# Performance work log

Measured on AMD Instinct MI355X. Metric: run time of the kernel, lower is better.

## Reference

```python
import jax, jax.numpy as jnp
import numpy as np

B, S, H = 2, 1024, 2048
NH, NKV, HD = 16, 4, 128
KB = 1024
THETA = 10000.0
NREP = NH // NKV
NEG = -1e9


def rotate_half(x):
    x1, x2 = x[..., : HD // 2], x[..., HD // 2 :]
    return jnp.concatenate((-x2, x1), axis=-1)


def setup_inputs() -> dict:
    key = jax.random.key(0)
    ks = jax.random.split(key, 9)
    wscale = 1.0 / np.sqrt(H)
    hidden_states = jax.random.normal(ks[0], (B, S, H), dtype=jnp.float32)
    # causal additive mask over the self-attention block only
    causal = jnp.tril(jnp.ones((S, S), dtype=bool))
    attention_mask = jnp.where(causal, 0.0, NEG).astype(jnp.float32)
    attention_mask = jnp.broadcast_to(attention_mask[None, None], (B, 1, S, S))
    position_ids = jnp.broadcast_to(jnp.arange(S, dtype=jnp.int32)[None], (B, S))
    kb_keys = jax.random.normal(ks[1], (B, KB, NKV * HD), dtype=jnp.float32)
    kb_values = jax.random.normal(ks[2], (B, KB, NKV * HD), dtype=jnp.float32)
    Wq = jax.random.normal(ks[3], (NH * HD, H), dtype=jnp.float32) * wscale
    Wq_new = jax.random.normal(ks[4], (NH * HD, H), dtype=jnp.float32) * wscale
    Wk = jax.random.normal(ks[5], (NKV * HD, H), dtype=jnp.float32) * wscale
    Wv = jax.random.normal(ks[6], (NKV * HD, H), dtype=jnp.float32) * wscale
    Wo = jax.random.normal(ks[7], (H, NH * HD), dtype=jnp.float32) * wscale
    return {
        'hidden_states': hidden_states, 'attention_mask': attention_mask,
        'position_ids': position_ids, 'kb_keys': kb_keys, 'kb_values': kb_values,
        'Wq': Wq, 'Wq_new': Wq_new, 'Wk': Wk, 'Wv': Wv, 'Wo': Wo,
    }


def _rope(position_ids, dtype):
    inv_freq = 1.0 / (THETA ** (jnp.arange(0, HD, 2, dtype=jnp.float32) / HD))
    freqs = position_ids.astype(jnp.float32)[:, :, None] * inv_freq[None, None, :]  # (B,S,HD/2)
    emb = jnp.concatenate((freqs, freqs), axis=-1)  # (B,S,HD)
    return jnp.cos(emb).astype(dtype)[:, None], jnp.sin(emb).astype(dtype)[:, None]  # (B,1,S,HD)


def reference(hidden_states, attention_mask, position_ids, kb_keys, kb_values,
              Wq, Wq_new, Wk, Wv, Wo):
    x = hidden_states
    q = jnp.einsum('bsh,dh->bsd', x, Wq).reshape(B, S, NH, HD).transpose(0, 2, 1, 3)
    q_new = jnp.einsum('bsh,dh->bsd', x, Wq_new).reshape(B, S, NH, HD).transpose(0, 2, 1, 3)
    k = jnp.einsum('bsh,dh->bsd', x, Wk).reshape(B, S, NKV, HD).transpose(0, 2, 1, 3)
    v = jnp.einsum('bsh,dh->bsd', x, Wv).reshape(B, S, NKV, HD).transpose(0, 2, 1, 3)

    cos, sin = _rope(position_ids, x.dtype)
    q = q * cos + rotate_half(q) * sin          # roped self queries
    k = k * cos + rotate_half(k) * sin          # roped self keys; q_new / KB keys stay un-roped

    # GQA repeat of KV heads
    k = jnp.repeat(k, NREP, axis=1)             # (B,NH,S,HD)
    v = jnp.repeat(v, NREP, axis=1)
    kb_k = jnp.repeat(kb_keys.reshape(B, KB, NKV, HD).transpose(0, 2, 1, 3), NREP, axis=1)   # (B,NH,KB,HD)
    kb_v = jnp.repeat(kb_values.reshape(B, KB, NKV, HD).transpose(0, 2, 1, 3), NREP, axis=1)

    scale = 1.0 / np.sqrt(HD)
    scores_kb = jnp.einsum('bhqd,bhkd->bhqk', q_new, kb_k) * scale      # (B,NH,S,KB)
    scores_self = jnp.einsum('bhqd,bhkd->bhqk', q, k) * scale + attention_mask  # (B,NH,S,S)
    scores = jnp.concatenate((scores_kb, scores_self), axis=-1)          # (B,NH,S,KB+S)
    attn = jax.nn.softmax(scores, axis=-1)

    v_full = jnp.concatenate((kb_v, v), axis=2)                          # (B,NH,KB+S,HD)
    out = jnp.einsum('bhqk,bhkd->bhqd', attn, v_full)                    # (B,NH,S,HD)
    out = out.transpose(0, 2, 1, 3).reshape(B, S, NH * HD)
    return jnp.einsum('bsd,hd->bsh', out, Wo)
```

## Files before the change

kernel.cpp:

```cpp
#include <hip/hip_runtime.h>

#define Bc   2
#define Sc   1024
#define Hc   2048
#define NHc  16
#define NKVc 4
#define HDc  128
#define KBc  1024
#define NREPc 4

typedef unsigned short ushort_t;
typedef unsigned int uint32;
typedef __attribute__((ext_vector_type(8))) __bf16 bf16x8;
typedef __attribute__((ext_vector_type(4))) float f32x4;

static __device__ __forceinline__ size_t dsz(int x) { return (size_t)x; }

static __device__ __forceinline__ ushort_t f2bf(float f) {
  uint32 u = __float_as_uint(f);
  u += 0x7fffu + ((u >> 16) & 1u);
  return (ushort_t)(u >> 16);
}
static __device__ __forceinline__ float bf2f(ushort_t u) {
  return __uint_as_float(((uint32)u) << 16);
}

#define ROPE_INV 0.14391156831212787f
#define QSCALE   (0.08838834764831845f * 1.4426950408889634f)

#define FSEG 1048576
__global__ void conv_all(const float* __restrict__ x,  const float* __restrict__ Wq,
                         const float* __restrict__ Wqn, const float* __restrict__ Wk,
                         const float* __restrict__ Wv,  const float* __restrict__ Wo,
                         ushort_t* xb, ushort_t* Wqb, ushort_t* Wqnb,
                         ushort_t* Wkb, ushort_t* Wvb, ushort_t* Wob)
{
  int i = blockIdx.x * 256 + threadIdx.x;
  const float* s; ushort_t* d; int off;
  if      (i <     FSEG)            { s = x;   d = xb;   off = i; }
  else if (i < 2 * FSEG)            { s = Wq;  d = Wqb;  off = i - FSEG; }
  else if (i < 3 * FSEG)            { s = Wqn; d = Wqnb; off = i - 2 * FSEG; }
  else if (i < 3 * FSEG + FSEG / 4) { s = Wk;  d = Wkb;  off = i - 3 * FSEG; }
  else if (i < 3 * FSEG + FSEG / 2) { s = Wv;  d = Wvb;  off = i - 3 * FSEG - FSEG / 4; }
  else                              { s = Wo;  d = Wob;  off = i - 3 * FSEG - FSEG / 2; }
  float4 v = ((const float4*)s)[off];
  ushort4 o;
  o.x = f2bf(v.x); o.y = f2bf(v.y); o.z = f2bf(v.z); o.w = f2bf(v.w);
  ((ushort4*)d)[off] = o;
}

#define GL16(gsrc, ldst)                                                \
  __builtin_amdgcn_global_load_lds(                                     \
      (const __attribute__((address_space(1))) void*)(gsrc),            \
      (__attribute__((address_space(3))) void*)(ldst), 16, 0, 0)

__global__ __launch_bounds__(256) void gemm_proj(
    const ushort_t* __restrict__ A,
    const ushort_t* __restrict__ Wqb,  const ushort_t* __restrict__ Wqnb,
    const ushort_t* __restrict__ Wkb,  const ushort_t* __restrict__ Wvb,
    ushort_t* __restrict__ qb, ushort_t* __restrict__ qnb,
    ushort_t* __restrict__ kkvb, ushort_t* __restrict__ vkvb)
{
  __shared__ ushort_t sA[128 * 32];
  __shared__ ushort_t sB[128 * 32];

  const int K = Hc;
  const int bx = blockIdx.x;
  const ushort_t* Bseg; ushort_t* Cseg; int segN, colseg; float scale;
  if      (bx < 16) { Bseg = Wqb;  Cseg = qb;   segN = 2048; colseg = bx * 128;        scale = 1.f; }
  else if (bx < 32) { Bseg = Wqnb; Cseg = qnb;  segN = 2048; colseg = (bx - 16) * 128; scale = QSCALE; }
  else if (bx < 36) { Bseg = Wkb;  Cseg = kkvb; segN = 512;  colseg = (bx - 32) * 128; scale = 1.f; }
  else              { Bseg = Wvb;  Cseg = vkvb; segN = 512;  colseg = (bx - 36) * 128; scale = 1.f; }

  const int tid  = threadIdx.x;
  const int lane = tid & 63;
  const int wid  = tid >> 6;
  const int wr   = wid >> 1;
  const int wc   = wid & 1;
  const int row0 = blockIdx.y * 128;
  const int fr = lane & 15;
  const int fq = lane >> 4;

  f32x4 acc[4][4];
  #pragma unroll
  for (int m = 0; m < 4; ++m)
    #pragma unroll
    for (int n = 0; n < 4; ++n) acc[m][n] = (f32x4){0.f, 0.f, 0.f, 0.f};

  const int rS = tid >> 2;
  const int kg = (tid & 3) * 8;
  const ushort_t* Asrc0 = A + dsz(row0 + rS) * K + kg;
  const ushort_t* Asrc1 = A + dsz(row0 + 64 + rS) * K + kg;
  const ushort_t* Bsrc0 = Bseg + dsz(colseg + rS) * K + kg;
  const ushort_t* Bsrc1 = Bseg + dsz(colseg + 64 + rS) * K + kg;
  char* ldsA0 = (char*)sA + tid * 16;
  char* ldsA1 = (char*)sA + 4096 + tid * 16;
  char* ldsB0 = (char*)sB + tid * 16;
  char* ldsB1 = (char*)sB + 4096 + tid * 16;

  for (int k0 = 0; k0 < K; k0 += 32) {
    GL16(Asrc0 + k0, ldsA0);
    GL16(Asrc1 + k0, ldsA1);
    GL16(Bsrc0 + k0, ldsB0);
    GL16(Bsrc1 + k0, ldsB1);
    __syncthreads();

    bf16x8 a[4], b[4];
    #pragma unroll
    for (int m = 0; m < 4; ++m)
      a[m] = *(const bf16x8*)&sA[(wr * 64 + m * 16 + fr) * 32 + fq * 8];
    #pragma unroll
    for (int n = 0; n < 4; ++n)
      b[n] = *(const bf16x8*)&sB[(wc * 64 + n * 16 + fr) * 32 + fq * 8];
    #pragma unroll
    for (int m = 0; m < 4; ++m)
      #pragma unroll
      for (int n = 0; n < 4; ++n)
        acc[m][n] = __builtin_amdgcn_mfma_f32_16x16x32_bf16(a[m], b[n], acc[m][n], 0, 0, 0);
    __syncthreads();
  }

  #pragma unroll
  for (int m = 0; m < 4; ++m)
    #pragma unroll
    for (int n = 0; n < 4; ++n)
      #pragma unroll
      for (int j = 0; j < 4; ++j)
        Cseg[dsz(row0 + wr * 64 + m * 16 + fq * 4 + j) * segN +
             colseg + wc * 64 + n * 16 + fr] = f2bf(acc[m][n][j] * scale);
}

__global__ __launch_bounds__(256) void gemm_bt_bf16(
    const ushort_t* __restrict__ A, const ushort_t* __restrict__ B,
    float* __restrict__ C, int M, int N, int K)
{
  __shared__ ushort_t sA[128 * 32];
  __shared__ ushort_t sB[128 * 32];

  const int tid  = threadIdx.x;
  const int lane = tid & 63;
  const int wid  = tid >> 6;
  const int wr   = wid >> 1;
  const int wc   = wid & 1;
  const int row0 = blockIdx.y * 128;
  const int col0 = blockIdx.x * 128;
  const int fr = lane & 15;
  const int fq = lane >> 4;

  f32x4 acc[4][4];
  #pragma unroll
  for (int m = 0; m < 4; ++m)
    #pragma unroll
    for (int n = 0; n < 4; ++n) acc[m][n] = (f32x4){0.f, 0.f, 0.f, 0.f};

  const int rS = tid >> 2;
  const int kg = (tid & 3) * 8;
  const ushort_t* Asrc0 = A + dsz(row0 + rS) * K + kg;
  const ushort_t* Asrc1 = A + dsz(row0 + 64 + rS) * K + kg;
  const ushort_t* Bsrc0 = B + dsz(col0 + rS) * K + kg;
  const ushort_t* Bsrc1 = B + dsz(col0 + 64 + rS) * K + kg;
  char* ldsA0 = (char*)sA + tid * 16;
  char* ldsA1 = (char*)sA + 4096 + tid * 16;
  char* ldsB0 = (char*)sB + tid * 16;
  char* ldsB1 = (char*)sB + 4096 + tid * 16;

  for (int k0 = 0; k0 < K; k0 += 32) {
    GL16(Asrc0 + k0, ldsA0);
    GL16(Asrc1 + k0, ldsA1);
    GL16(Bsrc0 + k0, ldsB0);
    GL16(Bsrc1 + k0, ldsB1);
    __syncthreads();

    bf16x8 a[4], b[4];
    #pragma unroll
    for (int m = 0; m < 4; ++m)
      a[m] = *(const bf16x8*)&sA[(wr * 64 + m * 16 + fr) * 32 + fq * 8];
    #pragma unroll
    for (int n = 0; n < 4; ++n)
      b[n] = *(const bf16x8*)&sB[(wc * 64 + n * 16 + fr) * 32 + fq * 8];
    #pragma unroll
    for (int m = 0; m < 4; ++m)
      #pragma unroll
      for (int n = 0; n < 4; ++n)
        acc[m][n] = __builtin_amdgcn_mfma_f32_16x16x32_bf16(a[m], b[n], acc[m][n], 0, 0, 0);
    __syncthreads();
  }

  #pragma unroll
  for (int m = 0; m < 4; ++m)
    #pragma unroll
    for (int n = 0; n < 4; ++n)
      #pragma unroll
      for (int j = 0; j < 4; ++j)
        C[dsz(row0 + wr * 64 + m * 16 + fq * 4 + j) * N +
          col0 + wc * 64 + n * 16 + fr] = acc[m][n][j];
}

__global__ void rope_q_ip(ushort_t* __restrict__ qb, const int* __restrict__ pos)
{
  int idx = blockIdx.x * blockDim.x + threadIdx.x;
  int j = idx & 63;
  int h = (idx >> 6) & 15;
  int r = idx >> 10;
  float p = (float)pos[r];
  float f = p * expf(-(float)j * ROPE_INV);
  float c = cosf(f), s = sinf(f);
  ushort_t* d = qb + dsz(r) * (NHc * HDc) + h * HDc;
  float x1 = bf2f(d[j]), x2 = bf2f(d[j + 64]);
  d[j]      = f2bf((x1 * c - x2 * s) * QSCALE);
  d[j + 64] = f2bf((x2 * c + x1 * s) * QSCALE);
}

__global__ void rope_k_kcat(const ushort_t* __restrict__ kkvb, const int* __restrict__ pos,
                            ushort_t* __restrict__ Kcat)
{
  int idx = blockIdx.x * blockDim.x + threadIdx.x;
  int j = idx & 63;
  int kvh = (idx >> 6) & 3;
  int s = (idx >> 8) & 1023;
  int b = idx >> 18;
  float p = (float)pos[b * Sc + s];
  float f = p * expf(-(float)j * ROPE_INV);
  float c = cosf(f), sn = sinf(f);
  const ushort_t* src = kkvb + dsz(b * Sc + s) * (NKVc * HDc) + kvh * HDc;
  ushort_t* dst = Kcat + (dsz(b * NKVc + kvh) * 2048 + 1024 + s) * HDc;
  float x1 = bf2f(src[j]), x2 = bf2f(src[j + 64]);
  dst[j]      = f2bf(x1 * c - x2 * sn);
  dst[j + 64] = f2bf(x2 * c + x1 * sn);
}

__global__ void kb_kcat(const float* __restrict__ src, ushort_t* __restrict__ Kcat)
{
  int i = blockIdx.x * blockDim.x + threadIdx.x;
  int d4 = i & 31;
  int kvh = (i >> 5) & 3;
  int k = (i >> 7) & 1023;
  int b = i >> 17;
  float4 v = *(const float4*)&src[dsz(b * KBc + k) * (NKVc * HDc) + kvh * HDc + d4 * 4];
  ushort4 o;
  o.x = f2bf(v.x); o.y = f2bf(v.y); o.z = f2bf(v.z); o.w = f2bf(v.w);
  *(ushort4*)&Kcat[(dsz(b * NKVc + kvh) * 2048 + k) * HDc + d4 * 4] = o;
}

__global__ __launch_bounds__(256) void vt_build(const float* __restrict__ kbv,
                                                const ushort_t* __restrict__ vkvb,
                                                ushort_t* __restrict__ Vt)
{
  __shared__ float sT[32][33];
  const int k0 = blockIdx.x * 32;
  const int d0 = blockIdx.y * 32;
  const int bk = blockIdx.z;
  const int b = bk >> 2, kvh = bk & 3;
  const int tid = threadIdx.x;

  #pragma unroll
  for (int t = 0; t < 4; ++t) {
    int li = tid + t * 256;
    int kk = li >> 5, dl = li & 31;
    int kg = k0 + kk;
    float v = (kg < 1024)
      ? kbv[dsz(b * KBc + kg) * (NKVc * HDc) + kvh * HDc + d0 + dl]
      : bf2f(vkvb[dsz(b * Sc + kg - 1024) * (NKVc * HDc) + kvh * HDc + d0 + dl]);
    sT[kk][dl] = v;
  }
  __syncthreads();
  #pragma unroll
  for (int t = 0; t < 4; ++t) {
    int li = tid + t * 256;
    int dl = li >> 5, kk = li & 31;
    Vt[(dsz(b * NKVc + kvh) * HDc + d0 + dl) * 2048 + k0 + kk] = f2bf(sT[kk][dl]);
  }
}

__global__ __launch_bounds__(256, 2) void attn_mfma3(
    const ushort_t* __restrict__ Qr,
    const ushort_t* __restrict__ Qn,
    const ushort_t* __restrict__ Kcat,
    const ushort_t* __restrict__ Vt,
    ushort_t* __restrict__ attnb)
{
  __shared__ ushort_t sK[2][32 * 128];
  __shared__ ushort_t sV[2][128 * 32];

  const int tid = threadIdx.x;
  const int lane = tid & 63;
  const int w = tid >> 6;
  const int fr = lane & 15;
  const int fq = lane >> 4;
  const int blk = blockIdx.x;
  const int qt = blk & 15;
  const int h  = (blk >> 4) & 15;
  const int b  = blk >> 8;
  const int kvh = h >> 2;
  const int qrow = qt * 64 + w * 16 + fr;
  const int kperm = ((fr >> 2) << 3) + (fr & 3);
  const int kswzU = (fr & 4) << 3;

  const ushort_t* Kb = Kcat + dsz(b * NKVc + kvh) * 2048 * HDc;
  const ushort_t* Vb = Vt   + dsz(b * NKVc + kvh) * HDc * 2048;

  const int kmask = (tid & 128) >> 1;
  const int kOff0 = (tid >> 4) * 256 + (((tid & 15) * 16) ^ kmask);
  const int vOff0 = (tid >> 2) * 4096 + (tid & 3) * 16;

  bf16x8 qn_f[4], qr_f[4];
  {
    const ushort_t* qn_row = Qn + dsz(b * Sc + qrow) * (NHc * HDc) + h * HDc;
    const ushort_t* qr_row = Qr + dsz(b * Sc + qrow) * (NHc * HDc) + h * HDc;
    #pragma unroll
    for (int c = 0; c < 4; ++c) {
      qn_f[c] = *(const bf16x8*)&qn_row[c * 32 + fq * 8];
      qr_f[c] = *(const bf16x8*)&qr_row[c * 32 + fq * 8];
    }
  }

  const int ntiles = (1119 + qt * 64) >> 5;

  float m = -1e30f, l = 0.f;
  f32x4 ot[8];
  #pragma unroll
  for (int dt = 0; dt < 8; ++dt) ot[dt] = (f32x4){0.f, 0.f, 0.f, 0.f};

#define STAGE(bi, t)                                                        \
  {                                                                         \
    const char* kg8 = (const char*)Kb + (size_t)(t) * 8192;                 \
    const char* vg8 = (const char*)Vb + (size_t)(t) * 64;                   \
    GL16(kg8 + kOff0,        (char*)&sK[bi][0] + tid * 16);                 \
    GL16(kg8 + kOff0 + 4096, (char*)&sK[bi][0] + 4096 + tid * 16);          \
    GL16(vg8 + vOff0,          (char*)&sV[bi][0] + tid * 16);               \
    GL16(vg8 + vOff0 + 262144, (char*)&sV[bi][0] + 4096 + tid * 16);        \
  }

  STAGE(0, 0);
  __syncthreads();

  for (int t = 0; t < ntiles; ++t) {
    const int cur = t & 1;
    if (t + 1 < ntiles) STAGE(cur ^ 1, t + 1);

    bf16x8 ka0[4], ka1[4], va[8];
    #pragma unroll
    for (int c = 0; c < 4; ++c) {
      ka0[c] = *(const bf16x8*)&sK[cur][kperm * 128 + ((c * 32 + fq * 8) ^ kswzU)];
      ka1[c] = *(const bf16x8*)&sK[cur][(kperm + 4) * 128 + ((c * 32 + fq * 8) ^ kswzU)];
    }
    #pragma unroll
    for (int dt = 0; dt < 8; ++dt)
      va[dt] = *(const bf16x8*)&sV[cur][(dt * 16 + fr) * 32 + fq * 8];

    f32x4 s0 = (f32x4){0.f, 0.f, 0.f, 0.f};
    f32x4 s1 = (f32x4){0.f, 0.f, 0.f, 0.f};
    const int kb = t * 32;
    if (kb < 1024) {
      #pragma unroll
      for (int c = 0; c < 4; ++c)
        s0 = __builtin_amdgcn_mfma_f32_16x16x32_bf16(ka0[c], qn_f[c], s0, 0, 0, 0);
      #pragma unroll
      for (int c = 0; c < 4; ++c)
        s1 = __builtin_amdgcn_mfma_f32_16x16x32_bf16(ka1[c], qn_f[c], s1, 0, 0, 0);
    } else {
      #pragma unroll
      for (int c = 0; c < 4; ++c)
        s0 = __builtin_amdgcn_mfma_f32_16x16x32_bf16(ka0[c], qr_f[c], s0, 0, 0, 0);
      #pragma unroll
      for (int c = 0; c < 4; ++c)
        s1 = __builtin_amdgcn_mfma_f32_16x16x32_bf16(ka1[c], qr_f[c], s1, 0, 0, 0);
      #pragma unroll
      for (int j = 0; j < 4; ++j) {
        s0[j] = (kb + fq * 8 + j     - 1024 > qrow) ? -1e30f : s0[j];
        s1[j] = (kb + fq * 8 + 4 + j - 1024 > qrow) ? -1e30f : s1[j];
      }
    }

    float tmax = fmaxf(fmaxf(fmaxf(s0[0], s0[1]), fmaxf(s0[2], s0[3])),
                       fmaxf(fmaxf(s1[0], s1[1]), fmaxf(s1[2], s1[3])));
    tmax = fmaxf(tmax, __shfl_xor(tmax, 16));
    tmax = fmaxf(tmax, __shfl_xor(tmax, 32));

    if (__any(tmax > m + 8.f)) {
      float mnew = fmaxf(m, tmax);
      float corr = exp2f(m - mnew);
      l *= corr;
      #pragma unroll
      for (int dt = 0; dt < 8; ++dt) {
        ot[dt][0] *= corr; ot[dt][1] *= corr;
        ot[dt][2] *= corr; ot[dt][3] *= corr;
      }
      m = mnew;
    }
    float ps = 0.f;
    bf16x8 pb;
    #pragma unroll
    for (int j = 0; j < 4; ++j) { float p = exp2f(s0[j] - m); ps += p; pb[j] = (__bf16)p; }
    #pragma unroll
    for (int j = 0; j < 4; ++j) { float p = exp2f(s1[j] - m); ps += p; pb[j + 4] = (__bf16)p; }
    l += ps;

    #pragma unroll
    for (int dt = 0; dt < 8; ++dt)
      ot[dt] = __builtin_amdgcn_mfma_f32_16x16x32_bf16(va[dt], pb, ot[dt], 0, 0, 0);

    __syncthreads();
  }
#undef STAGE

  l += __shfl_xor(l, 16);
  l += __shfl_xor(l, 32);
  const float linv = 1.f / l;
  ushort_t* obase = attnb + dsz(b * Sc + qrow) * (NHc * HDc) + h * HDc;
  #pragma unroll
  for (int dt = 0; dt < 8; ++dt) {
    ushort_t o4a[4];
    #pragma unroll
    for (int j = 0; j < 4; ++j) o4a[j] = f2bf(ot[dt][j] * linv);
    *(ushort4*)&obase[dt * 16 + fq * 4] = *(ushort4*)o4a;
  }
}

extern "C" void kernel_launch(void* const* d_in, const int* in_sizes, int n_in,
                              void* d_out, int out_size, void* d_ws, size_t ws_size,
                              hipStream_t stream)
{
  const float* x    = (const float*)d_in[0];
  const int*   pos  = (const int*)d_in[2];
  const float* kbk  = (const float*)d_in[3];
  const float* kbv  = (const float*)d_in[4];
  const float* Wq   = (const float*)d_in[5];
  const float* Wqn  = (const float*)d_in[6];
  const float* Wk   = (const float*)d_in[7];
  const float* Wv   = (const float*)d_in[8];
  const float* Wo   = (const float*)d_in[9];
  float* out = (float*)d_out;

  const int MR = Bc * Sc;
  const size_t MU = 1048576;

  ushort_t* U = (ushort_t*)d_ws;
  ushort_t* xb    = U;
  ushort_t* Wqb   = U + 4  * MU;
  ushort_t* Wqnb  = U + 8  * MU;
  ushort_t* Wkb   = U + 12 * MU;
  ushort_t* Wvb   = U + 13 * MU;
  ushort_t* Wob   = U + 14 * MU;
  ushort_t* qb    = U + 18 * MU;
  ushort_t* qnb   = U + 22 * MU;
  ushort_t* kkvb  = U + 26 * MU;
  ushort_t* vkvb  = U + 27 * MU;
  ushort_t* Kcat  = U + 28 * MU;
  ushort_t* Vt    = U + 30 * MU;
  ushort_t* attnb = U + 32 * MU;

  dim3 blk(256);

  conv_all<<<18432, blk, 0, stream>>>(x, Wq, Wqn, Wk, Wv, Wo,
                                      xb, Wqb, Wqnb, Wkb, Wvb, Wob);
  gemm_proj<<<dim3(40, 16), blk, 0, stream>>>(xb, Wqb, Wqnb, Wkb, Wvb,
                                              qb, qnb, kkvb, vkvb);
  rope_q_ip<<<8192, blk, 0, stream>>>(qb, pos);
  kb_kcat<<<1024, blk, 0, stream>>>(kbk, Kcat);
  rope_k_kcat<<<2048, blk, 0, stream>>>(kkvb, pos, Kcat);
  vt_build<<<dim3(64, 4, 8), blk, 0, stream>>>(kbv, vkvb, Vt);
  attn_mfma3<<<512, blk, 0, stream>>>(qb, qnb, Kcat, Vt, attnb);
  gemm_bt_bf16<<<dim3(16, 16), blk, 0, stream>>>(attnb, Wob, out, MR, 2048, Hc);
}
```

Measured before the change: 224.5 us.

## Process two query row-blocks per wave in attention kernel with 128-thread blocks

```diff
diff --git a/kernel.cpp b/kernel.cpp
--- a/kernel.cpp
+++ b/kernel.cpp
@@ -272,7 +272,7 @@
   }
 }
 
-__global__ __launch_bounds__(256, 2) void attn_mfma3(
+__global__ __launch_bounds__(128) void attn_mfma4(
     const ushort_t* __restrict__ Qr,
     const ushort_t* __restrict__ Qn,
     const ushort_t* __restrict__ Kcat,
@@ -292,43 +292,54 @@
   const int h  = (blk >> 4) & 15;
   const int b  = blk >> 8;
   const int kvh = h >> 2;
-  const int qrow = qt * 64 + w * 16 + fr;
   const int kperm = ((fr >> 2) << 3) + (fr & 3);
-  const int kswzU = (fr & 4) << 3;
 
   const ushort_t* Kb = Kcat + dsz(b * NKVc + kvh) * 2048 * HDc;
   const ushort_t* Vb = Vt   + dsz(b * NKVc + kvh) * HDc * 2048;
 
-  const int kmask = (tid & 128) >> 1;
-  const int kOff0 = (tid >> 4) * 256 + (((tid & 15) * 16) ^ kmask);
-  const int vOff0 = (tid >> 2) * 4096 + (tid & 3) * 16;
-
-  bf16x8 qn_f[4], qr_f[4];
+  const int qrow0 = qt * 64 + w * 32 + fr;
+  const int qrow1 = qrow0 + 16;
+  const int vslot = (fq ^ ((fr >> 1) & 3)) * 8;
+
+  const int ntiles = 34 + 2 * qt;
+
+  float m0 = -1e30f, l0 = 0.f, m1 = -1e30f, l1 = 0.f;
+  f32x4 ot0[8], ot1[8];
+  #pragma unroll
+  for (int dt = 0; dt < 8; ++dt) {
+    ot0[dt] = (f32x4){0.f, 0.f, 0.f, 0.f};
+    ot1[dt] = (f32x4){0.f, 0.f, 0.f, 0.f};
+  }
+
+#define STAGE(bi, t)                                                     \
+  {                                                                      \
+    const char* kgb = (const char*)Kb + (size_t)(t) * 8192;              \
+    const char* vgb = (const char*)Vb + (size_t)(t) * 64;                \
+    _Pragma("unroll")                                                    \
+    for (int cc = 0; cc < 4; ++cc) {                                     \
+      int r  = cc * 8 + (tid >> 4);                                      \
+      int uu = (r & 3) | ((r >> 3) << 2);                                \
+      GL16(kgb + r * 256 + (((tid & 15) ^ uu) * 16),                     \
+           (char*)&sK[bi][0] + cc * 2048 + tid * 16);                    \
+    }                                                                    \
+    _Pragma("unroll")                                                    \
+    for (int cc = 0; cc < 4; ++cc) {                                     \
+      int r  = cc * 32 + (tid >> 2);                                     \
+      int uv = (r >> 1) & 3;                                             \
+      GL16(vgb + (size_t)r * 4096 + (((tid & 3) ^ uv) * 16),             \
+           (char*)&sV[bi][0] + cc * 2048 + tid * 16);                    \
+    }                                                                    \
+  }
+
+  bf16x8 qf0[4], qf1[4];
   {
-    const ushort_t* qn_row = Qn + dsz(b * Sc + qrow) * (NHc * HDc) + h * HDc;
-    const ushort_t* qr_row = Qr + dsz(b * Sc + qrow) * (NHc * HDc) + h * HDc;
+    const ushort_t* p0 = Qn + dsz(b * Sc + qrow0) * (NHc * HDc) + h * HDc;
+    const ushort_t* p1 = Qn + dsz(b * Sc + qrow1) * (NHc * HDc) + h * HDc;
     #pragma unroll
     for (int c = 0; c < 4; ++c) {
-      qn_f[c] = *(const bf16x8*)&qn_row[c * 32 + fq * 8];
-      qr_f[c] = *(const bf16x8*)&qr_row[c * 32 + fq * 8];
+      qf0[c] = *(const bf16x8*)&p0[c * 32 + fq * 8];
+      qf1[c] = *(const bf16x8*)&p1[c * 32 + fq * 8];
     }
-  }
-
-  const int ntiles = (1119 + qt * 64) >> 5;
-
-  float m = -1e30f, l = 0.f;
-  f32x4 ot[8];
-  #pragma unroll
-  for (int dt = 0; dt < 8; ++dt) ot[dt] = (f32x4){0.f, 0.f, 0.f, 0.f};
-
-#define STAGE(bi, t)                                                        \
-  {                                                                         \
-    const char* kg8 = (const char*)Kb + (size_t)(t) * 8192;                 \
-    const char* vg8 = (const char*)Vb + (size_t)(t) * 64;                   \
-    GL16(kg8 + kOff0,        (char*)&sK[bi][0] + tid * 16);                 \
-    GL16(kg8 + kOff0 + 4096, (char*)&sK[bi][0] + 4096 + tid * 16);          \
-    GL16(vg8 + vOff0,          (char*)&sV[bi][0] + tid * 16);               \
-    GL16(vg8 + vOff0 + 262144, (char*)&sV[bi][0] + 4096 + tid * 16);        \
   }
 
   STAGE(0, 0);
@@ -338,82 +349,140 @@
     const int cur = t & 1;
     if (t + 1 < ntiles) STAGE(cur ^ 1, t + 1);
 
-    bf16x8 ka0[4], ka1[4], va[8];
-    #pragma unroll
-    for (int c = 0; c < 4; ++c) {
-      ka0[c] = *(const bf16x8*)&sK[cur][kperm * 128 + ((c * 32 + fq * 8) ^ kswzU)];
-      ka1[c] = *(const bf16x8*)&sK[cur][(kperm + 4) * 128 + ((c * 32 + fq * 8) ^ kswzU)];
-    }
-    #pragma unroll
-    for (int dt = 0; dt < 8; ++dt)
-      va[dt] = *(const bf16x8*)&sV[cur][(dt * 16 + fr) * 32 + fq * 8];
-
-    f32x4 s0 = (f32x4){0.f, 0.f, 0.f, 0.f};
-    f32x4 s1 = (f32x4){0.f, 0.f, 0.f, 0.f};
-    const int kb = t * 32;
-    if (kb < 1024) {
-      #pragma unroll
-      for (int c = 0; c < 4; ++c)
-        s0 = __builtin_amdgcn_mfma_f32_16x16x32_bf16(ka0[c], qn_f[c], s0, 0, 0, 0);
-      #pragma unroll
-      for (int c = 0; c < 4; ++c)
-        s1 = __builtin_amdgcn_mfma_f32_16x16x32_bf16(ka1[c], qn_f[c], s1, 0, 0, 0);
-    } else {
-      #pragma unroll
-      for (int c = 0; c < 4; ++c)
-        s0 = __builtin_amdgcn_mfma_f32_16x16x32_bf16(ka0[c], qr_f[c], s0, 0, 0, 0);
-      #pragma unroll
-      for (int c = 0; c < 4; ++c)
-        s1 = __builtin_amdgcn_mfma_f32_16x16x32_bf16(ka1[c], qr_f[c], s1, 0, 0, 0);
-      #pragma unroll
-      for (int j = 0; j < 4; ++j) {
-        s0[j] = (kb + fq * 8 + j     - 1024 > qrow) ? -1e30f : s0[j];
-        s1[j] = (kb + fq * 8 + 4 + j - 1024 > qrow) ? -1e30f : s1[j];
+    if (t == 32) {
+      const ushort_t* p0 = Qr + dsz(b * Sc + qrow0) * (NHc * HDc) + h * HDc;
+      const ushort_t* p1 = Qr + dsz(b * Sc + qrow1) * (NHc * HDc) + h * HDc;
+      #pragma unroll
+      for (int c = 0; c < 4; ++c) {
+        qf0[c] = *(const bf16x8*)&p0[c * 32 + fq * 8];
+        qf1[c] = *(const bf16x8*)&p1[c * 32 + fq * 8];
       }
     }
-
-    float tmax = fmaxf(fmaxf(fmaxf(s0[0], s0[1]), fmaxf(s0[2], s0[3])),
-                       fmaxf(fmaxf(s1[0], s1[1]), fmaxf(s1[2], s1[3])));
-    tmax = fmaxf(tmax, __shfl_xor(tmax, 16));
-    tmax = fmaxf(tmax, __shfl_xor(tmax, 32));
-
-    if (__any(tmax > m + 8.f)) {
-      float mnew = fmaxf(m, tmax);
-      float corr = exp2f(m - mnew);
-      l *= corr;
-      #pragma unroll
-      for (int dt = 0; dt < 8; ++dt) {
-        ot[dt][0] *= corr; ot[dt][1] *= corr;
-        ot[dt][2] *= corr; ot[dt][3] *= corr;
+    const bool self = (t >= 32);
+
+    bf16x8 ka0[4], ka1[4], va[8];
+    #pragma unroll
+    for (int c = 0; c < 4; ++c) {
+      const int ks = ((c * 4 + fq) ^ fr) * 8;
+      ka0[c] = *(const bf16x8*)&sK[cur][kperm * 128 + ks];
+      ka1[c] = *(const bf16x8*)&sK[cur][(kperm + 4) * 128 + ks];
+    }
+    #pragma unroll
+    for (int dt = 0; dt < 8; ++dt)
+      va[dt] = *(const bf16x8*)&sV[cur][(dt * 16 + fr) * 32 + vslot];
+
+    {
+      f32x4 s0 = (f32x4){0.f, 0.f, 0.f, 0.f};
+      f32x4 s1 = (f32x4){0.f, 0.f, 0.f, 0.f};
+      __builtin_amdgcn_s_setprio(1);
+      #pragma unroll
+      for (int c = 0; c < 4; ++c)
+        s0 = __builtin_amdgcn_mfma_f32_16x16x32_bf16(ka0[c], qf0[c], s0, 0, 0, 0);
+      #pragma unroll
+      for (int c = 0; c < 4; ++c)
+        s1 = __builtin_amdgcn_mfma_f32_16x16x32_bf16(ka1[c], qf0[c], s1, 0, 0, 0);
+      __builtin_amdgcn_s_setprio(0);
+      if (self) {
+        #pragma unroll
+        for (int j = 0; j < 4; ++j) {
+          s0[j] = (t * 32 + fq * 8 + j     - 1024 > qrow0) ? -1e30f : s0[j];
+          s1[j] = (t * 32 + fq * 8 + 4 + j - 1024 > qrow0) ? -1e30f : s1[j];
+        }
       }
-      m = mnew;
+      float tmax = fmaxf(fmaxf(fmaxf(s0[0], s0[1]), fmaxf(s0[2], s0[3])),
+                         fmaxf(fmaxf(s1[0], s1[1]), fmaxf(s1[2], s1[3])));
+      tmax = fmaxf(tmax, __shfl_xor(tmax, 16));
+      tmax = fmaxf(tmax, __shfl_xor(tmax, 32));
+      if (__any(tmax > m0 + 8.f)) {
+        float mnew = fmaxf(m0, tmax);
+        float corr = exp2f(m0 - mnew);
+        l0 *= corr;
+        #pragma unroll
+        for (int dt = 0; dt < 8; ++dt) {
+          ot0[dt][0] *= corr; ot0[dt][1] *= corr;
+          ot0[dt][2] *= corr; ot0[dt][3] *= corr;
+        }
+        m0 = mnew;
+      }
+      float ps = 0.f;
+      bf16x8 pb;
+      #pragma unroll
+      for (int j = 0; j < 4; ++j) { float p = exp2f(s0[j] - m0); ps += p; pb[j] = (__bf16)p; }
+      #pragma unroll
+      for (int j = 0; j < 4; ++j) { float p = exp2f(s1[j] - m0); ps += p; pb[j + 4] = (__bf16)p; }
+      l0 += ps;
+      __builtin_amdgcn_s_setprio(1);
+      #pragma unroll
+      for (int dt = 0; dt < 8; ++dt)
+        ot0[dt] = __builtin_amdgcn_mfma_f32_16x16x32_bf16(va[dt], pb, ot0[dt], 0, 0, 0);
+      __builtin_amdgcn_s_setprio(0);
     }
-    float ps = 0.f;
-    bf16x8 pb;
-    #pragma unroll
-    for (int j = 0; j < 4; ++j) { float p = exp2f(s0[j] - m); ps += p; pb[j] = (__bf16)p; }
-    #pragma unroll
-    for (int j = 0; j < 4; ++j) { float p = exp2f(s1[j] - m); ps += p; pb[j + 4] = (__bf16)p; }
-    l += ps;
-
-    #pragma unroll
-    for (int dt = 0; dt < 8; ++dt)
-      ot[dt] = __builtin_amdgcn_mfma_f32_16x16x32_bf16(va[dt], pb, ot[dt], 0, 0, 0);
+    {
+      f32x4 s0 = (f32x4){0.f, 0.f, 0.f, 0.f};
+      f32x4 s1 = (f32x4){0.f, 0.f, 0.f, 0.f};
+      __builtin_amdgcn_s_setprio(1);
+      #pragma unroll
+      for (int c = 0; c < 4; ++c)
+        s0 = __builtin_amdgcn_mfma_f32_16x16x32_bf16(ka0[c], qf1[c], s0, 0, 0, 0);
+      #pragma unroll
+      for (int c = 0; c < 4; ++c)
+        s1 = __builtin_amdgcn_mfma_f32_16x16x32_bf16(ka1[c], qf1[c], s1, 0, 0, 0);
+      __builtin_amdgcn_s_setprio(0);
+      if (self) {
+        #pragma unroll
+        for (int j = 0; j < 4; ++j) {
+          s0[j] = (t * 32 + fq * 8 + j     - 1024 > qrow1) ? -1e30f : s0[j];
+          s1[j] = (t * 32 + fq * 8 + 4 + j - 1024 > qrow1) ? -1e30f : s1[j];
+        }
+      }
+      float tmax = fmaxf(fmaxf(fmaxf(s0[0], s0[1]), fmaxf(s0[2], s0[3])),
+                         fmaxf(fmaxf(s1[0], s1[1]), fmaxf(s1[2], s1[3])));
+      tmax = fmaxf(tmax, __shfl_xor(tmax, 16));
+      tmax = fmaxf(tmax, __shfl_xor(tmax, 32));
+      if (__any(tmax > m1 + 8.f)) {
+        float mnew = fmaxf(m1, tmax);
+        float corr = exp2f(m1 - mnew);
+        l1 *= corr;
+        #pragma unroll
+        for (int dt = 0; dt < 8; ++dt) {
+          ot1[dt][0] *= corr; ot1[dt][1] *= corr;
+          ot1[dt][2] *= corr; ot1[dt][3] *= corr;
+        }
+        m1 = mnew;
+      }
+      float ps = 0.f;
+      bf16x8 pb;
+      #pragma unroll
+      for (int j = 0; j < 4; ++j) { float p = exp2f(s0[j] - m1); ps += p; pb[j] = (__bf16)p; }
+      #pragma unroll
+      for (int j = 0; j < 4; ++j) { float p = exp2f(s1[j] - m1); ps += p; pb[j + 4] = (__bf16)p; }
+      l1 += ps;
+      __builtin_amdgcn_s_setprio(1);
+      #pragma unroll
+      for (int dt = 0; dt < 8; ++dt)
+        ot1[dt] = __builtin_amdgcn_mfma_f32_16x16x32_bf16(va[dt], pb, ot1[dt], 0, 0, 0);
+      __builtin_amdgcn_s_setprio(0);
+    }
 
     __syncthreads();
   }
 #undef STAGE
 
-  l += __shfl_xor(l, 16);
-  l += __shfl_xor(l, 32);
-  const float linv = 1.f / l;
-  ushort_t* obase = attnb + dsz(b * Sc + qrow) * (NHc * HDc) + h * HDc;
+  l0 += __shfl_xor(l0, 16); l0 += __shfl_xor(l0, 32);
+  l1 += __shfl_xor(l1, 16); l1 += __shfl_xor(l1, 32);
+  const float li0 = 1.f / l0;
+  const float li1 = 1.f / l1;
+  ushort_t* ob0 = attnb + dsz(b * Sc + qrow0) * (NHc * HDc) + h * HDc;
+  ushort_t* ob1 = attnb + dsz(b * Sc + qrow1) * (NHc * HDc) + h * HDc;
   #pragma unroll
   for (int dt = 0; dt < 8; ++dt) {
     ushort_t o4a[4];
     #pragma unroll
-    for (int j = 0; j < 4; ++j) o4a[j] = f2bf(ot[dt][j] * linv);
-    *(ushort4*)&obase[dt * 16 + fq * 4] = *(ushort4*)o4a;
+    for (int j = 0; j < 4; ++j) o4a[j] = f2bf(ot0[dt][j] * li0);
+    *(ushort4*)&ob0[dt * 16 + fq * 4] = *(ushort4*)o4a;
+    #pragma unroll
+    for (int j = 0; j < 4; ++j) o4a[j] = f2bf(ot1[dt][j] * li1);
+    *(ushort4*)&ob1[dt * 16 + fq * 4] = *(ushort4*)o4a;
   }
 }
 
@@ -460,6 +529,6 @@
   kb_kcat<<<1024, blk, 0, stream>>>(kbk, Kcat);
   rope_k_kcat<<<2048, blk, 0, stream>>>(kkvb, pos, Kcat);
   vt_build<<<dim3(64, 4, 8), blk, 0, stream>>>(kbv, vkvb, Vt);
-  attn_mfma3<<<512, blk, 0, stream>>>(qb, qnb, Kcat, Vt, attnb);
+  attn_mfma4<<<512, dim3(128), 0, stream>>>(qb, qnb, Kcat, Vt, attnb);
   gemm_bt_bf16<<<dim3(16, 16), blk, 0, stream>>>(attnb, Wob, out, MR, 2048, Hc);
 }
```

Result: slower. 245.2 us (+9.2%).

## Split attention KV range in two per query tile and merge partials

Applied to the files above, without the earlier changes.

```diff
diff --git a/kernel.cpp b/kernel.cpp
--- a/kernel.cpp
+++ b/kernel.cpp
@@ -272,12 +272,13 @@
   }
 }
 
-__global__ __launch_bounds__(256, 2) void attn_mfma3(
+__global__ __launch_bounds__(256, 4) void attn_mfma5(
     const ushort_t* __restrict__ Qr,
     const ushort_t* __restrict__ Qn,
     const ushort_t* __restrict__ Kcat,
     const ushort_t* __restrict__ Vt,
-    ushort_t* __restrict__ attnb)
+    ushort_t* __restrict__ Opart,
+    float* __restrict__ mlpart)
 {
   __shared__ ushort_t sK[2][32 * 128];
   __shared__ ushort_t sV[2][128 * 32];
@@ -288,90 +289,98 @@
   const int fr = lane & 15;
   const int fq = lane >> 4;
   const int blk = blockIdx.x;
+  const int half = blockIdx.y;
   const int qt = blk & 15;
   const int h  = (blk >> 4) & 15;
   const int b  = blk >> 8;
   const int kvh = h >> 2;
   const int qrow = qt * 64 + w * 16 + fr;
   const int kperm = ((fr >> 2) << 3) + (fr & 3);
-  const int kswzU = (fr & 4) << 3;
 
   const ushort_t* Kb = Kcat + dsz(b * NKVc + kvh) * 2048 * HDc;
   const ushort_t* Vb = Vt   + dsz(b * NKVc + kvh) * HDc * 2048;
 
-  const int kmask = (tid & 128) >> 1;
-  const int kOff0 = (tid >> 4) * 256 + (((tid & 15) * 16) ^ kmask);
-  const int vOff0 = (tid >> 2) * 4096 + (tid & 3) * 16;
-
-  bf16x8 qn_f[4], qr_f[4];
+  const int nt  = 34 + 2 * qt;
+  const int mid = nt >> 1;
+  const int t_lo = half ? mid : 0;
+  const int t_hi = half ? nt  : mid;
+
+  const int kr0 = tid >> 4;
+  const int ks0 = tid & 15;
+  const int ku0 = (kr0 & 3) | ((kr0 >> 3) << 2);
+  const int kOffA = kr0 * 256 + ((ks0 ^ ku0) * 16);
+  const int kOffB = (kr0 + 16) * 256 + ((ks0 ^ (ku0 + 8)) * 16);
+  const int vr0 = tid >> 2;
+  const int vs0 = tid & 3;
+  const int vu0 = (vr0 >> 1) & 3;
+  const size_t vOffA = (size_t)vr0 * 4096 + ((vs0 ^ vu0) * 16);
+  const size_t vOffB = vOffA + (size_t)64 * 4096;
+
+  const int vslot = (fq ^ ((fr >> 1) & 3)) * 8;
+
+#define STAGE(bi, t)                                                   \
+  {                                                                    \
+    const char* kgb = (const char*)Kb + (size_t)(t) * 8192;            \
+    const char* vgb = (const char*)Vb + (size_t)(t) * 64;              \
+    GL16(kgb + kOffA, (char*)&sK[bi][0] + tid * 16);                   \
+    GL16(kgb + kOffB, (char*)&sK[bi][0] + 4096 + tid * 16);            \
+    GL16(vgb + vOffA, (char*)&sV[bi][0] + tid * 16);                   \
+    GL16(vgb + vOffB, (char*)&sV[bi][0] + 4096 + tid * 16);            \
+  }
+
+  bf16x8 qf[4];
   {
-    const ushort_t* qn_row = Qn + dsz(b * Sc + qrow) * (NHc * HDc) + h * HDc;
-    const ushort_t* qr_row = Qr + dsz(b * Sc + qrow) * (NHc * HDc) + h * HDc;
-    #pragma unroll
-    for (int c = 0; c < 4; ++c) {
-      qn_f[c] = *(const bf16x8*)&qn_row[c * 32 + fq * 8];
-      qr_f[c] = *(const bf16x8*)&qr_row[c * 32 + fq * 8];
-    }
-  }
-
-  const int ntiles = (1119 + qt * 64) >> 5;
+    const ushort_t* qp = (t_lo >= 32 ? Qr : Qn) + dsz(b * Sc + qrow) * (NHc * HDc) + h * HDc;
+    #pragma unroll
+    for (int c = 0; c < 4; ++c) qf[c] = *(const bf16x8*)&qp[c * 32 + fq * 8];
+  }
 
   float m = -1e30f, l = 0.f;
   f32x4 ot[8];
   #pragma unroll
   for (int dt = 0; dt < 8; ++dt) ot[dt] = (f32x4){0.f, 0.f, 0.f, 0.f};
 
-#define STAGE(bi, t)                                                        \
-  {                                                                         \
-    const char* kg8 = (const char*)Kb + (size_t)(t) * 8192;                 \
-    const char* vg8 = (const char*)Vb + (size_t)(t) * 64;                   \
-    GL16(kg8 + kOff0,        (char*)&sK[bi][0] + tid * 16);                 \
-    GL16(kg8 + kOff0 + 4096, (char*)&sK[bi][0] + 4096 + tid * 16);          \
-    GL16(vg8 + vOff0,          (char*)&sV[bi][0] + tid * 16);               \
-    GL16(vg8 + vOff0 + 262144, (char*)&sV[bi][0] + 4096 + tid * 16);        \
-  }
-
-  STAGE(0, 0);
+  STAGE(0, t_lo);
   __syncthreads();
 
-  for (int t = 0; t < ntiles; ++t) {
-    const int cur = t & 1;
-    if (t + 1 < ntiles) STAGE(cur ^ 1, t + 1);
+  for (int t = t_lo; t < t_hi; ++t) {
+    const int cur = (t - t_lo) & 1;
+    if (t + 1 < t_hi) STAGE(cur ^ 1, t + 1);
+
+    if (t == 32) {
+      const ushort_t* qp = Qr + dsz(b * Sc + qrow) * (NHc * HDc) + h * HDc;
+      #pragma unroll
+      for (int c = 0; c < 4; ++c) qf[c] = *(const bf16x8*)&qp[c * 32 + fq * 8];
+    }
+    const bool self = (t >= 32);
 
     bf16x8 ka0[4], ka1[4], va[8];
     #pragma unroll
     for (int c = 0; c < 4; ++c) {
-      ka0[c] = *(const bf16x8*)&sK[cur][kperm * 128 + ((c * 32 + fq * 8) ^ kswzU)];
-      ka1[c] = *(const bf16x8*)&sK[cur][(kperm + 4) * 128 + ((c * 32 + fq * 8) ^ kswzU)];
+      const int ks = ((c * 4 + fq) ^ fr) * 8;
+      ka0[c] = *(const bf16x8*)&sK[cur][kperm * 128 + ks];
+      ka1[c] = *(const bf16x8*)&sK[cur][(kperm + 4) * 128 + ks];
     }
     #pragma unroll
     for (int dt = 0; dt < 8; ++dt)
-      va[dt] = *(const bf16x8*)&sV[cur][(dt * 16 + fr) * 32 + fq * 8];
+      va[dt] = *(const bf16x8*)&sV[cur][(dt * 16 + fr) * 32 + vslot];
 
     f32x4 s0 = (f32x4){0.f, 0.f, 0.f, 0.f};
     f32x4 s1 = (f32x4){0.f, 0.f, 0.f, 0.f};
-    const int kb = t * 32;
-    if (kb < 1024) {
-      #pragma unroll
-      for (int c = 0; c < 4; ++c)
-        s0 = __builtin_amdgcn_mfma_f32_16x16x32_bf16(ka0[c], qn_f[c], s0, 0, 0, 0);
-      #pragma unroll
-      for (int c = 0; c < 4; ++c)
-        s1 = __builtin_amdgcn_mfma_f32_16x16x32_bf16(ka1[c], qn_f[c], s1, 0, 0, 0);
-    } else {
-      #pragma unroll
-      for (int c = 0; c < 4; ++c)
-        s0 = __builtin_amdgcn_mfma_f32_16x16x32_bf16(ka0[c], qr_f[c], s0, 0, 0, 0);
-      #pragma unroll
-      for (int c = 0; c < 4; ++c)
-        s1 = __builtin_amdgcn_mfma_f32_16x16x32_bf16(ka1[c], qr_f[c], s1, 0, 0, 0);
+    #pragma unroll
+    for (int c = 0; c < 4; ++c)
+      s0 = __builtin_amdgcn_mfma_f32_16x16x32_bf16(ka0[c], qf[c], s0, 0, 0, 0);
+    #pragma unroll
+    for (int c = 0; c < 4; ++c)
+      s1 = __builtin_amdgcn_mfma_f32_16x16x32_bf16(ka1[c], qf[c], s1, 0, 0, 0);
+
+    if (self) {
       #pragma unroll
       for (int j = 0; j < 4; ++j) {
-        s0[j] = (kb + fq * 8 + j     - 1024 > qrow) ? -1e30f : s0[j];
-        s1[j] = (kb + fq * 8 + 4 + j - 1024 > qrow) ? -1e30f : s1[j];
+        s0[j] = (t * 32 + fq * 8 + j     - 1024 > qrow) ? -1e30f : s0[j];
+        s1[j] = (t * 32 + fq * 8 + 4 + j - 1024 > qrow) ? -1e30f : s1[j];
       }
     }
-
     float tmax = fmaxf(fmaxf(fmaxf(s0[0], s0[1]), fmaxf(s0[2], s0[3])),
                        fmaxf(fmaxf(s1[0], s1[1]), fmaxf(s1[2], s1[3])));
     tmax = fmaxf(tmax, __shfl_xor(tmax, 16));
@@ -406,15 +415,66 @@
 
   l += __shfl_xor(l, 16);
   l += __shfl_xor(l, 32);
-  const float linv = 1.f / l;
-  ushort_t* obase = attnb + dsz(b * Sc + qrow) * (NHc * HDc) + h * HDc;
+
+  const int qin = w * 16 + fr;
+  ushort_t* ob = Opart + (dsz(half * 512 + blk) * 64 + qin) * 128;
   #pragma unroll
   for (int dt = 0; dt < 8; ++dt) {
     ushort_t o4a[4];
     #pragma unroll
-    for (int j = 0; j < 4; ++j) o4a[j] = f2bf(ot[dt][j] * linv);
-    *(ushort4*)&obase[dt * 16 + fq * 4] = *(ushort4*)o4a;
-  }
+    for (int j = 0; j < 4; ++j) o4a[j] = f2bf(ot[dt][j]);
+    *(ushort4*)&ob[dt * 16 + fq * 4] = *(ushort4*)o4a;
+  }
+  if (fq == 0) {
+    float* mlp = mlpart + (dsz(half * 512 + blk) * 64 + qin) * 2;
+    mlp[0] = m;
+    mlp[1] = l;
+  }
+}
+
+__global__ void attn_merge(const ushort_t* __restrict__ Opart,
+                           const float* __restrict__ mlpart,
+                           ushort_t* __restrict__ attnb)
+{
+  const int i = blockIdx.x * 256 + threadIdx.x;
+  const int e = i * 8;
+  const int qg = e >> 7;
+  const int d0 = e & 127;
+  const int blk = qg >> 6;
+  const int qin = qg & 63;
+  const int qt = blk & 15;
+  const int h  = (blk >> 4) & 15;
+  const int b  = blk >> 8;
+
+  const float* ml0 = mlpart + dsz(blk) * 128 + qin * 2;
+  const float* ml1 = mlpart + dsz(512 + blk) * 128 + qin * 2;
+  const float m0 = ml0[0], l0 = ml0[1];
+  const float m1 = ml1[0], l1 = ml1[1];
+  const float M = fmaxf(m0, m1);
+  const float s0 = exp2f(m0 - M), s1 = exp2f(m1 - M);
+  const float Linv = 1.f / (l0 * s0 + l1 * s1);
+  const float c0 = s0 * Linv, c1 = s1 * Linv;
+
+  const ushort_t* o0 = Opart + (dsz(blk) * 64 + qin) * 128 + d0;
+  const ushort_t* o1 = Opart + (dsz(512 + blk) * 64 + qin) * 128 + d0;
+  ushort4 a0 = *(const ushort4*)&o0[0];
+  ushort4 b0 = *(const ushort4*)&o1[0];
+  ushort4 a1 = *(const ushort4*)&o0[4];
+  ushort4 b1 = *(const ushort4*)&o1[4];
+
+  ushort_t r[8];
+  r[0] = f2bf(bf2f(a0.x) * c0 + bf2f(b0.x) * c1);
+  r[1] = f2bf(bf2f(a0.y) * c0 + bf2f(b0.y) * c1);
+  r[2] = f2bf(bf2f(a0.z) * c0 + bf2f(b0.z) * c1);
+  r[3] = f2bf(bf2f(a0.w) * c0 + bf2f(b0.w) * c1);
+  r[4] = f2bf(bf2f(a1.x) * c0 + bf2f(b1.x) * c1);
+  r[5] = f2bf(bf2f(a1.y) * c0 + bf2f(b1.y) * c1);
+  r[6] = f2bf(bf2f(a1.z) * c0 + bf2f(b1.z) * c1);
+  r[7] = f2bf(bf2f(a1.w) * c0 + bf2f(b1.w) * c1);
+
+  ushort_t* dst = attnb + dsz(b * Sc + qt * 64 + qin) * (NHc * HDc) + h * HDc + d0;
+  *(ushort4*)&dst[0] = *(ushort4*)&r[0];
+  *(ushort4*)&dst[4] = *(ushort4*)&r[4];
 }
 
 extern "C" void kernel_launch(void* const* d_in, const int* in_sizes, int n_in,
@@ -449,6 +509,8 @@
   ushort_t* Kcat  = U + 28 * MU;
   ushort_t* Vt    = U + 30 * MU;
   ushort_t* attnb = U + 32 * MU;
+  ushort_t* Opart  = U;
+  float*    mlpart = (float*)(U + 26 * MU);
 
   dim3 blk(256);
 
@@ -460,6 +522,7 @@
   kb_kcat<<<1024, blk, 0, stream>>>(kbk, Kcat);
   rope_k_kcat<<<2048, blk, 0, stream>>>(kkvb, pos, Kcat);
   vt_build<<<dim3(64, 4, 8), blk, 0, stream>>>(kbv, vkvb, Vt);
-  attn_mfma3<<<512, blk, 0, stream>>>(qb, qnb, Kcat, Vt, attnb);
+  attn_mfma5<<<dim3(512, 2), blk, 0, stream>>>(qb, qnb, Kcat, Vt, Opart, mlpart);
+  attn_merge<<<2048, blk, 0, stream>>>(Opart, mlpart, attnb);
   gemm_bt_bf16<<<dim3(16, 16), blk, 0, stream>>>(attnb, Wob, out, MR, 2048, Hc);
 }
```

Result: faster. 198.3 us (-11.7%).
